# Kernel tuning notes

Measured on AMD Instinct MI355X. Metric: run time of the kernel, lower is better.

Reference implementation:

```python
import jax, jax.numpy as jnp
import numpy as np

C = 512
G = 4
CG = C // G            # 128 channels per group
R = max(1, CG // 8)    # 16 reduced dim per group
TOPK = max(1, int(C * 0.75))  # 384
TAU = 0.5
ALPHA = 0.1
EPS = 1e-8


def setup_inputs() -> dict:
    key = jax.random.key(0)
    k1, k2, k3, k4, k5, k6 = jax.random.split(key, 6)
    B, H, W = 16, 112, 112
    x = jax.random.normal(k1, (B, C, H, W), dtype=jnp.float32)
    noise_u = jax.random.uniform(k2, (B, C), dtype=jnp.float32)
    # grouped MLP params: Linear(2*CG -> R), ReLU, Linear(R -> CG), stacked over G
    W1 = jax.random.normal(k3, (G, 2 * CG, R), dtype=jnp.float32) * 0.05
    b1 = jax.random.normal(k4, (G, R), dtype=jnp.float32) * 0.05
    W2 = jax.random.normal(k5, (G, R, CG), dtype=jnp.float32) * 0.05
    b2 = jax.random.normal(k6, (G, CG), dtype=jnp.float32) * 0.05
    return {"x": x, "W1": W1, "b1": b1, "W2": W2, "b2": b2, "noise_u": noise_u}


def reference(x, W1, b1, W2, b2, noise_u):
    B = x.shape[0]
    # channel SE pooling: avg + max over HxW -> [B, C] each
    avg_pooled = jnp.mean(x, axis=(2, 3))
    max_pooled = jnp.max(x, axis=(2, 3))
    combined = jnp.concatenate([avg_pooled, max_pooled], axis=1)  # [B, 2C]
    # torch.chunk of the 2C vector into G groups (mixed avg/max slices)
    gf = combined.reshape(B, G, 2 * CG)  # [B, G, 2*CG]
    h = jax.nn.relu(jnp.einsum('bgi,gir->bgr', gf, W1) + b1)      # [B, G, R]
    score = (jnp.einsum('bgr,gro->bgo', h, W2) + b2).reshape(B, C)  # [B, C]
    # hard top-k mask
    _, topk_idx = jax.lax.top_k(score, TOPK)                      # [B, TOPK]
    hard_mask = jnp.zeros((B, C), dtype=score.dtype).at[
        jnp.arange(B)[:, None], topk_idx].set(1.0)
    # gumbel-sigmoid soft score (training branch)
    gumbel = -jnp.log(-jnp.log(noise_u + EPS) + EPS)
    soft = jax.nn.sigmoid((score + gumbel) / TAU)
    mask = hard_mask * soft                                        # [B, C]
    # residual blend: x*mask + x*(1-mask)*alpha
    blend = mask + (1.0 - mask) * ALPHA
    return x * blend[:, :, None, None]
```

## Files before the change

kernel.cpp:

```cpp
#include <hip/hip_runtime.h>
#include <math.h>

#define NC   512
#define NG   4
#define NCG  128
#define NR   16
#define NTOPK 384
#define NB   16
#define HW   (112 * 112)
#define NV4  (HW / 4)
#define ALPHA 0.1f
#define EPSC  1e-8f

typedef float f32x4 __attribute__((ext_vector_type(4)));

__global__ __launch_bounds__(256) void pool_kernel(
    const float* __restrict__ x, float* __restrict__ avg_out,
    float* __restrict__ max_out) {
  const int bc = blockIdx.x;
  const f32x4* p = reinterpret_cast<const f32x4*>(x + (size_t)bc * HW);
  float s = 0.f;
  float m = -INFINITY;
  for (int i = threadIdx.x; i < 3072; i += 1024) {
    f32x4 v0 = p[i];
    f32x4 v1 = p[i + 256];
    f32x4 v2 = p[i + 512];
    f32x4 v3 = p[i + 768];
    s += (v0.x + v0.y) + (v0.z + v0.w);
    s += (v1.x + v1.y) + (v1.z + v1.w);
    s += (v2.x + v2.y) + (v2.z + v2.w);
    s += (v3.x + v3.y) + (v3.z + v3.w);
    m = fmaxf(m, fmaxf(fmaxf(v0.x, v0.y), fmaxf(v0.z, v0.w)));
    m = fmaxf(m, fmaxf(fmaxf(v1.x, v1.y), fmaxf(v1.z, v1.w)));
    m = fmaxf(m, fmaxf(fmaxf(v2.x, v2.y), fmaxf(v2.z, v2.w)));
    m = fmaxf(m, fmaxf(fmaxf(v3.x, v3.y), fmaxf(v3.z, v3.w)));
  }
  if (threadIdx.x < 64) {
    f32x4 v = p[3072 + threadIdx.x];
    s += (v.x + v.y) + (v.z + v.w);
    m = fmaxf(m, fmaxf(fmaxf(v.x, v.y), fmaxf(v.z, v.w)));
  }
  #pragma unroll
  for (int off = 32; off > 0; off >>= 1) {
    s += __shfl_down(s, off, 64);
    m = fmaxf(m, __shfl_down(m, off, 64));
  }
  __shared__ float ss[4], sm[4];
  const int wave = threadIdx.x >> 6;
  const int lane = threadIdx.x & 63;
  if (lane == 0) { ss[wave] = s; sm[wave] = m; }
  __syncthreads();
  if (threadIdx.x == 0) {
    float st = (ss[0] + ss[1]) + (ss[2] + ss[3]);
    float mt = fmaxf(fmaxf(sm[0], sm[1]), fmaxf(sm[2], sm[3]));
    avg_out[bc] = st / (float)HW;
    max_out[bc] = mt;
  }
}

__global__ __launch_bounds__(256) void fused_kernel(
    const float* __restrict__ x, const float* __restrict__ avg,
    const float* __restrict__ mx, const float* __restrict__ W1,
    const float* __restrict__ b1, const float* __restrict__ W2,
    const float* __restrict__ b2, const float* __restrict__ noise_u,
    float* __restrict__ out) {
  const int rb = 1023 - (int)blockIdx.x;
  const int b  = rb >> 6;
  const int c0 = (rb & 63) * 8;
  const int t  = threadIdx.x;

  __shared__ float comb[2 * NC];
  __shared__ float h[NG * NR];
  __shared__ float sc[NC];
  __shared__ float blend_loc[8];

  {
    const float* pa = avg + b * NC;
    const float* pm = mx  + b * NC;
    comb[t]             = pa[t];
    comb[t + 256]       = pa[t + 256];
    comb[512 + t]       = pm[t];
    comb[512 + t + 256] = pm[t + 256];
  }
  __syncthreads();

  {
    const int pair = t >> 2, sub = t & 3;
    const int g = pair >> 4, r = pair & 15;
    const float* cf = comb + g * (2 * NCG);
    const float* w  = W1 + (size_t)g * (2 * NCG) * NR + r;
    const int i0 = sub * 64;
    float acc = 0.f;
    #pragma unroll 8
    for (int i = 0; i < 64; ++i) acc += cf[i0 + i] * w[(i0 + i) * NR];
    acc += __shfl_down(acc, 2, 4);
    acc += __shfl_down(acc, 1, 4);
    if (sub == 0) h[pair] = fmaxf(acc + b1[g * NR + r], 0.f);
  }
  __syncthreads();

  #pragma unroll
  for (int cc = 0; cc < 2; ++cc) {
    const int c = t + cc * 256;
    const int g = c >> 7, o = c & 127;
    float acc = b2[g * NCG + o];
    const float* w  = W2 + (size_t)g * NR * NCG + o;
    const float* hh = h + g * NR;
    #pragma unroll
    for (int r = 0; r < NR; ++r) acc += hh[r] * w[r * NCG];
    sc[c] = acc;
  }
  __syncthreads();

  {
    const int ci = t >> 5, sub = t & 31;
    const int c = c0 + ci;
    const float my = sc[c];
    int cnt = 0;
    const int j0 = sub * 16;
    #pragma unroll
    for (int jj = 0; jj < 16; ++jj) {
      const int j = j0 + jj;
      const float v = sc[j];
      cnt += (v > my) || (v == my && j < c);
    }
    cnt += __shfl_down(cnt, 16, 32);
    cnt += __shfl_down(cnt,  8, 32);
    cnt += __shfl_down(cnt,  4, 32);
    cnt += __shfl_down(cnt,  2, 32);
    cnt += __shfl_down(cnt,  1, 32);
    if (sub == 0) {
      const float hard = (cnt < NTOPK) ? 1.f : 0.f;
      const float u = noise_u[b * NC + c];
      const float gum = -logf(-logf(u + EPSC) + EPSC);
      const float soft = 1.f / (1.f + expf(-(my + gum) * 2.0f));
      const float mask = hard * soft;
      blend_loc[ci] = mask + (1.f - mask) * ALPHA;
    }
  }
  __syncthreads();

  for (int k = 7; k >= 0; --k) {
    const int bc = rb * 8 + k;
    const float s = blend_loc[k];
    const f32x4* p = reinterpret_cast<const f32x4*>(x + (size_t)bc * HW);
    f32x4* q = reinterpret_cast<f32x4*>(out + (size_t)bc * HW);
    for (int i = t; i < 3072; i += 1024) {
      f32x4 v0 = p[i];
      f32x4 v1 = p[i + 256];
      f32x4 v2 = p[i + 512];
      f32x4 v3 = p[i + 768];
      v0 *= s; v1 *= s; v2 *= s; v3 *= s;
      __builtin_nontemporal_store(v0, &q[i]);
      __builtin_nontemporal_store(v1, &q[i + 256]);
      __builtin_nontemporal_store(v2, &q[i + 512]);
      __builtin_nontemporal_store(v3, &q[i + 768]);
    }
    if (t < 64) {
      const int i = 3072 + t;
      f32x4 v = p[i];
      v *= s;
      __builtin_nontemporal_store(v, &q[i]);
    }
  }
}

extern "C" void kernel_launch(void* const* d_in, const int* in_sizes, int n_in,
                              void* d_out, int out_size, void* d_ws, size_t ws_size,
                              hipStream_t stream) {
  const float* x       = (const float*)d_in[0];
  const float* W1      = (const float*)d_in[1];
  const float* b1      = (const float*)d_in[2];
  const float* W2      = (const float*)d_in[3];
  const float* b2      = (const float*)d_in[4];
  const float* noise_u = (const float*)d_in[5];
  float* out = (float*)d_out;

  float* ws_avg = (float*)d_ws;
  float* ws_max = ws_avg + NB * NC;

  pool_kernel<<<NB * NC, 256, 0, stream>>>(x, ws_avg, ws_max);
  fused_kernel<<<1024, 256, 0, stream>>>(x, ws_avg, ws_max, W1, b1, W2, b2,
                                         noise_u, out);
}
```

Measured before the change: 217.0 us.

## Pipeline pooling and scaling over batch chunks to reuse x in cache

Splits the batch into four chunks and launches combined kernels that scale chunk ch while pooling chunk ch+1, so the second read of each chunk's x may hit the last-level cache. This replaces the single full pool pass followed by a full scale pass. It adds extra launches and mixes two block roles in one grid, and cache residency of the roughly 100 MB chunks is not guaranteed.

```diff
diff --git a/kernel.cpp b/kernel.cpp
--- a/kernel.cpp
+++ b/kernel.cpp
@@ -1,27 +1,32 @@
 #include <hip/hip_runtime.h>
 #include <math.h>
 
-#define NC   512
-#define NG   4
-#define NCG  128
-#define NR   16
+#define NC    512
+#define NG    4
+#define NCG   128
+#define NR    16
 #define NTOPK 384
-#define NB   16
-#define HW   (112 * 112)
-#define NV4  (HW / 4)
+#define NB    16
+#define HW    (112 * 112)
 #define ALPHA 0.1f
 #define EPSC  1e-8f
 
+#define CHUNK      4
+#define NCHUNK     (NB / CHUNK)
+#define BC_PER_CH  (CHUNK * NC)
+#define SCALE_BLKS (CHUNK * 64)
+
 typedef float f32x4 __attribute__((ext_vector_type(4)));
 
-__global__ __launch_bounds__(256) void pool_kernel(
-    const float* __restrict__ x, float* __restrict__ avg_out,
-    float* __restrict__ max_out) {
-  const int bc = blockIdx.x;
+__device__ __forceinline__ void pool_one(const float* __restrict__ x, int bc,
+                                         float* __restrict__ avg_out,
+                                         float* __restrict__ max_out,
+                                         float* ss, float* sm) {
+  const int t = threadIdx.x;
   const f32x4* p = reinterpret_cast<const f32x4*>(x + (size_t)bc * HW);
   float s = 0.f;
   float m = -INFINITY;
-  for (int i = threadIdx.x; i < 3072; i += 1024) {
+  for (int i = t; i < 3072; i += 1024) {
     f32x4 v0 = p[i];
     f32x4 v1 = p[i + 256];
     f32x4 v2 = p[i + 512];
@@ -35,8 +40,8 @@
     m = fmaxf(m, fmaxf(fmaxf(v2.x, v2.y), fmaxf(v2.z, v2.w)));
     m = fmaxf(m, fmaxf(fmaxf(v3.x, v3.y), fmaxf(v3.z, v3.w)));
   }
-  if (threadIdx.x < 64) {
-    f32x4 v = p[3072 + threadIdx.x];
+  if (t < 64) {
+    f32x4 v = p[3072 + t];
     s += (v.x + v.y) + (v.z + v.w);
     m = fmaxf(m, fmaxf(fmaxf(v.x, v.y), fmaxf(v.z, v.w)));
   }
@@ -45,12 +50,10 @@
     s += __shfl_down(s, off, 64);
     m = fmaxf(m, __shfl_down(m, off, 64));
   }
-  __shared__ float ss[4], sm[4];
-  const int wave = threadIdx.x >> 6;
-  const int lane = threadIdx.x & 63;
+  const int wave = t >> 6, lane = t & 63;
   if (lane == 0) { ss[wave] = s; sm[wave] = m; }
   __syncthreads();
-  if (threadIdx.x == 0) {
+  if (t == 0) {
     float st = (ss[0] + ss[1]) + (ss[2] + ss[3]);
     float mt = fmaxf(fmaxf(sm[0], sm[1]), fmaxf(sm[2], sm[3]));
     avg_out[bc] = st / (float)HW;
@@ -58,21 +61,16 @@
   }
 }
 
-__global__ __launch_bounds__(256) void fused_kernel(
-    const float* __restrict__ x, const float* __restrict__ avg,
+__device__ __forceinline__ void scale_part(
+    int ch, int rb, const float* __restrict__ x, const float* __restrict__ avg,
     const float* __restrict__ mx, const float* __restrict__ W1,
     const float* __restrict__ b1, const float* __restrict__ W2,
     const float* __restrict__ b2, const float* __restrict__ noise_u,
-    float* __restrict__ out) {
-  const int rb = 1023 - (int)blockIdx.x;
-  const int b  = rb >> 6;
+    float* __restrict__ out, float* comb, float* sc, float* h,
+    float* blend_loc) {
+  const int b  = ch * CHUNK + (rb >> 6);
   const int c0 = (rb & 63) * 8;
   const int t  = threadIdx.x;
-
-  __shared__ float comb[2 * NC];
-  __shared__ float h[NG * NR];
-  __shared__ float sc[NC];
-  __shared__ float blend_loc[8];
 
   {
     const float* pa = avg + b * NC;
@@ -140,8 +138,8 @@
   }
   __syncthreads();
 
-  for (int k = 7; k >= 0; --k) {
-    const int bc = rb * 8 + k;
+  for (int k = 0; k < 8; ++k) {
+    const int bc = (b * NC) + c0 + k;
     const float s = blend_loc[k];
     const f32x4* p = reinterpret_cast<const f32x4*>(x + (size_t)bc * HW);
     f32x4* q = reinterpret_cast<f32x4*>(out + (size_t)bc * HW);
@@ -165,6 +163,34 @@
   }
 }
 
+__global__ __launch_bounds__(256) void pool_kernel(
+    const float* __restrict__ x, float* __restrict__ avg_out,
+    float* __restrict__ max_out) {
+  __shared__ float ss[4], sm[4];
+  pool_one(x, blockIdx.x, avg_out, max_out, ss, sm);
+}
+
+__global__ __launch_bounds__(256) void combo_kernel(
+    const float* __restrict__ x, float* __restrict__ avg,
+    float* __restrict__ mx, const float* __restrict__ W1,
+    const float* __restrict__ b1, const float* __restrict__ W2,
+    const float* __restrict__ b2, const float* __restrict__ noise_u,
+    float* __restrict__ out, int ch) {
+  __shared__ float comb[2 * NC];
+  __shared__ float sc[NC];
+  __shared__ float h[NG * NR];
+  __shared__ float blend_loc[8];
+  __shared__ float ss[4], sm[4];
+
+  if (blockIdx.x < SCALE_BLKS) {
+    scale_part(ch, blockIdx.x, x, avg, mx, W1, b1, W2, b2, noise_u, out,
+               comb, sc, h, blend_loc);
+  } else {
+    const int bc = (ch + 1) * BC_PER_CH + ((int)blockIdx.x - SCALE_BLKS);
+    pool_one(x, bc, avg, mx, ss, sm);
+  }
+}
+
 extern "C" void kernel_launch(void* const* d_in, const int* in_sizes, int n_in,
                               void* d_out, int out_size, void* d_ws, size_t ws_size,
                               hipStream_t stream) {
@@ -179,7 +205,10 @@
   float* ws_avg = (float*)d_ws;
   float* ws_max = ws_avg + NB * NC;
 
-  pool_kernel<<<NB * NC, 256, 0, stream>>>(x, ws_avg, ws_max);
-  fused_kernel<<<1024, 256, 0, stream>>>(x, ws_avg, ws_max, W1, b1, W2, b2,
-                                         noise_u, out);
-}
+  pool_kernel<<<BC_PER_CH, 256, 0, stream>>>(x, ws_avg, ws_max);
+  for (int ch = 0; ch < NCHUNK; ++ch) {
+    const int nblk = (ch + 1 < NCHUNK) ? (SCALE_BLKS + BC_PER_CH) : SCALE_BLKS;
+    combo_kernel<<<nblk, 256, 0, stream>>>(x, ws_avg, ws_max, W1, b1, W2, b2,
+                                           noise_u, out, ch);
+  }
+}
```

Measured after the change: 231.3 us. 6.6% more time.
